# Kernel tuning notes

Measured on AMD Instinct MI355X. Metric: run time of the kernel, lower is better.

## Reference

```python
import jax, jax.numpy as jnp
import numpy as np

B, L, D = 4, 2048, 256
H, HD = 8, 64
MAX_LEN = 2048


def setup_inputs() -> dict:
    key = jax.random.key(0)
    ks = jax.random.split(key, 5)
    x = jax.random.normal(ks[0], (B, L, D), dtype=jnp.float32)
    glorot_q = (2.0 / (D + H * HD)) ** 0.5
    Wq = jax.random.normal(ks[1], (D, H * HD), dtype=jnp.float32) * glorot_q
    Wk = jax.random.normal(ks[2], (D, H * HD), dtype=jnp.float32) * glorot_q
    bq = jnp.zeros((H, 1, 1, HD), dtype=jnp.float32)
    bk = jnp.zeros((H, 1, 1, HD), dtype=jnp.float32)
    prior_mean = jax.random.uniform(ks[3], (H,), dtype=jnp.float32, minval=-1.0, maxval=1.0)
    log_prior_std = jnp.full((H,), np.log(0.4), dtype=jnp.float32)
    return {"x": x, "Wq": Wq, "bq": bq, "Wk": Wk, "bk": bk,
            "prior_mean": prior_mean, "log_prior_std": log_prior_std,
            "max_length": MAX_LEN}


def _gaussian(x, mean, std):
    return 1.0 / std / jnp.sqrt(2.0 * 3.1415926) * jnp.exp(-0.5 * (x - mean) ** 2 / std ** 2)


def reference(x, Wq, bq, Wk, bk, prior_mean, log_prior_std, max_length):
    b, l, d = x.shape
    h, hd = bq.shape[0], bq.shape[-1]
    # normalized signed distance matrix [l, l]
    r = jnp.arange(l, dtype=jnp.float32)
    dist = (r[None, :] - r[:, None]) / float(max_length)
    # projections -> [h, b, l, hd] (split heads along last dim, heads leading)
    q = (x @ Wq).reshape(b, l, h, hd).transpose(2, 0, 1, 3) + bq
    k = (x @ Wk).reshape(b, l, h, hd).transpose(2, 0, 1, 3) + bk
    # gaussian positional prior per head [h, l, l]
    prior = _gaussian(dist[None, :, :], prior_mean[:, None, None],
                      jnp.exp(log_prior_std)[:, None, None])
    # scaled QK^T * prior -> softmax over keys
    scores = jnp.einsum('hbqd,hbkd->hbqk', q, k) * (float(hd) ** -0.5)
    att = jax.nn.softmax(scores * prior[:, None, :, :], axis=-1)
    # distance-weighted reduction instead of V-matmul: [h, b, l] -> [b, l, h]
    distance = jnp.einsum('hbqk,qk->hbq', att, dist)
    return distance.transpose(1, 2, 0)
```

## Files before the change

kernel.cpp:

```cpp
#include <hip/hip_runtime.h>
#include <math.h>


#define B_  4
#define L_  2048
#define D_  256
#define H_  8
#define HD_ 64

typedef unsigned int u32;
typedef unsigned short u16;
typedef short bf16x8 __attribute__((ext_vector_type(8)));
typedef float f32x4  __attribute__((ext_vector_type(4)));

__device__ __forceinline__ u16 bf16rne(float v) {
    u32 u = __float_as_uint(v);
    return (u16)((u + 0x7fffu + ((u >> 16) & 1u)) >> 16);
}
__device__ __forceinline__ float bf2f(u16 h) { return __uint_as_float(((u32)h) << 16); }

#if __has_builtin(__builtin_amdgcn_exp2f)
__device__ __forceinline__ float fast_exp2(float x) { return __builtin_amdgcn_exp2f(x); }
#else
__device__ __forceinline__ float fast_exp2(float x) { return exp2f(x); }
#endif

__global__ __launch_bounds__(256, 4) void projB_kernel(
    const float* __restrict__ x,
    const float* __restrict__ Wq, const float* __restrict__ bq,
    const float* __restrict__ Wk, const float* __restrict__ bk,
    u16* __restrict__ Qhi, u16* __restrict__ Qlo,
    u16* __restrict__ Khi, u16* __restrict__ Klo)
{
    __shared__ __align__(16) u16 Bs[2][64][40];

    const int z = blockIdx.z;
    const float* W    = z ? Wk : Wq;
    const float* bias = z ? bk : bq;
    u16* Ohi = z ? Khi : Qhi;
    u16* Olo = z ? Klo : Qlo;

    const int t = threadIdx.x, w = t >> 6, l = t & 63;
    const int kc = l & 15, lhi = l >> 4;
    const int m0 = blockIdx.x * 128 + w * 32;
    const int h  = blockIdx.y;

    const float* xp0 = x + (size_t)(m0 + kc) * D_;
    const float* xp1 = x + (size_t)(m0 + 16 + kc) * D_;

    f32x4 acc[2][4];
    #pragma unroll
    for (int mf = 0; mf < 2; ++mf)
        #pragma unroll
        for (int nf = 0; nf < 4; ++nf) acc[mf][nf] = (f32x4){0.f, 0.f, 0.f, 0.f};

    for (int ks = 0; ks < 8; ++ks) {
        __syncthreads();
        #pragma unroll
        for (int j = 0; j < 2; ++j) {
            const int fid = t + j * 256;
            const int kr = fid >> 4, c4 = fid & 15;
            float4 v = *(const float4*)&W[(size_t)(ks*32 + kr) * 512 + h*64 + c4*4];
            float vv[4] = {v.x, v.y, v.z, v.w};
            #pragma unroll
            for (int e = 0; e < 4; ++e) {
                const int n = c4*4 + e;
                const u16 hi = bf16rne(vv[e]);
                Bs[0][n][kr] = hi;
                Bs[1][n][kr] = bf16rne(vv[e] - bf2f(hi));
            }
        }
        __syncthreads();

        union { u16 u[8]; bf16x8 v; } ah[2], al[2];
        #pragma unroll
        for (int mf = 0; mf < 2; ++mf) {
            const float* xp = mf ? xp1 : xp0;
            float4 a = *(const float4*)(xp + ks*32 + lhi*8);
            float4 b = *(const float4*)(xp + ks*32 + lhi*8 + 4);
            float vv[8] = {a.x, a.y, a.z, a.w, b.x, b.y, b.z, b.w};
            #pragma unroll
            for (int e = 0; e < 8; ++e) {
                const u16 hi = bf16rne(vv[e]);
                ah[mf].u[e] = hi;
                al[mf].u[e] = bf16rne(vv[e] - bf2f(hi));
            }
        }

        #pragma unroll
        for (int nf = 0; nf < 4; ++nf) {
            const bf16x8 bh = *(const bf16x8*)&Bs[0][nf*16 + kc][lhi*8];
            const bf16x8 bl = *(const bf16x8*)&Bs[1][nf*16 + kc][lhi*8];
            #pragma unroll
            for (int mf = 0; mf < 2; ++mf) {
                acc[mf][nf] = __builtin_amdgcn_mfma_f32_16x16x32_bf16(ah[mf].v, bh, acc[mf][nf], 0, 0, 0);
                acc[mf][nf] = __builtin_amdgcn_mfma_f32_16x16x32_bf16(ah[mf].v, bl, acc[mf][nf], 0, 0, 0);
                acc[mf][nf] = __builtin_amdgcn_mfma_f32_16x16x32_bf16(al[mf].v, bh, acc[mf][nf], 0, 0, 0);
            }
        }
    }

    #pragma unroll
    for (int mf = 0; mf < 2; ++mf)
        #pragma unroll
        for (int nf = 0; nf < 4; ++nf) {
            const float bv = bias[h * 64 + nf*16 + kc];
            #pragma unroll
            for (int r = 0; r < 4; ++r) {
                const float v = acc[mf][nf][r] + bv;
                const u16 hi = bf16rne(v);
                const u16 lo = bf16rne(v - bf2f(hi));
                const int m = m0 + mf*16 + lhi*4 + r;
                const int bb = m >> 11, ll = m & (L_ - 1);
                const size_t o = (((size_t)h * B_ + bb) * L_ + ll) * HD_ + nf*16 + kc;
                Ohi[o] = hi; Olo[o] = lo;
            }
        }
}

__global__ __launch_bounds__(512, 2) void attn_kernel(
    const u16* __restrict__ Qhi, const u16* __restrict__ Qlo,
    const u16* __restrict__ Khi, const u16* __restrict__ Klo,
    const float* __restrict__ prior_mean, const float* __restrict__ log_prior_std,
    const int* __restrict__ max_len, float* __restrict__ out)
{
    __shared__ __align__(16) u16 kls[2][2][64 * 64];

    const int t = threadIdx.x, w = t >> 6, l = t & 63;
    const int kc = l & 15, lhi = l >> 4;

    const int p = blockIdx.x;
    const int xcd = p & 7, s = p >> 3;
    const int hb = xcd * 4 + (s >> 3);
    const int q0 = (s & 7) * 256;
    const int h = hb >> 2, b = hb & 3;
    const int qw = q0 + w * 32;

    const float iml = 1.0f / (float)(*max_len);
    const float mu  = prior_mean[h];
    const float sg  = __expf(log_prior_std[h]);
    const float isg = 1.0f / sg;
    const float S2  = 0.84932180f;
    const float A2  = iml * isg * S2;
    const float B2  = -mu * isg * S2;
    const float LC  = __log2f(0.125f * 1.44269504089f / (sg * 2.5066282746310002f));

    bf16x8 qh[2][2], ql2[2][2];
    #pragma unroll
    for (int qf = 0; qf < 2; ++qf)
        #pragma unroll
        for (int dh = 0; dh < 2; ++dh) {
            const size_t qo = ((size_t)hb * L_ + qw + qf*16 + kc) * HD_ + dh*32 + lhi*8;
            qh[qf][dh]  = *(const bf16x8*)&Qhi[qo];
            ql2[qf][dh] = *(const bf16x8*)&Qlo[qo];
        }

    const int d0q0 = lhi*4 - (q0 + w*32 + kc);
    const int d0q1 = d0q0 - 16;

    const int spl = t >> 8;
    const int srow = (t & 255) >> 2;
    const int sq = t & 3;
    const int sr7 = srow & 7;
    const u16* Kg = (spl ? Klo : Khi) + ((size_t)hb * L_ + srow) * HD_ + sq * 16;
    const int p0 = ((sq*2)     ^ sr7) * 8;
    const int p1 = ((sq*2 + 1) ^ sr7) * 8;
    u16* wdst0 = &kls[0][spl][srow * 64];
    u16* wdst1 = &kls[1][spl][srow * 64];

    const int sl0 = (lhi ^ (kc & 7)) * 8;
    const int sl1 = ((4 + lhi) ^ (kc & 7)) * 8;

    float lv0 = 0.f, wv0 = 0.f, lv1 = 0.f, wv1 = 0.f;

    uint4 ra0, ra1, rb0, rb1;
    ra0 = *(const uint4*)Kg; ra1 = *(const uint4*)(Kg + 8);
    *(uint4*)&wdst0[p0] = ra0; *(uint4*)&wdst0[p1] = ra1;
    ra0 = *(const uint4*)(Kg + 4096); ra1 = *(const uint4*)(Kg + 4096 + 8);
    __syncthreads();

#define LOADT(RX0, RX1, TI) { const u16* src_ = Kg + (size_t)(TI) * 4096; \
    RX0 = *(const uint4*)src_; RX1 = *(const uint4*)(src_ + 8); }
#define WRT(DST, RX0, RX1) { *(uint4*)&DST[p0] = RX0; *(uint4*)&DST[p1] = RX1; }
#define CTILE(TI, BS) { \
    const u16* bh_ = &kls[BS][0][0]; const u16* bl_ = &kls[BS][1][0]; \
    f32x4 acc[4][2]; \
    _Pragma("unroll") for (int kf = 0; kf < 4; ++kf) { \
        acc[kf][0] = (f32x4){0.f,0.f,0.f,0.f}; acc[kf][1] = (f32x4){0.f,0.f,0.f,0.f}; } \
    __builtin_amdgcn_s_setprio(1); \
    _Pragma("unroll") for (int kf = 0; kf < 4; ++kf) { \
        const int rb_ = (kf*16 + kc) * 64; \
        const bf16x8 ah0 = *(const bf16x8*)&bh_[rb_ + sl0]; \
        const bf16x8 ah1 = *(const bf16x8*)&bh_[rb_ + sl1]; \
        const bf16x8 al0 = *(const bf16x8*)&bl_[rb_ + sl0]; \
        const bf16x8 al1 = *(const bf16x8*)&bl_[rb_ + sl1]; \
        _Pragma("unroll") for (int qf = 0; qf < 2; ++qf) { \
            acc[kf][qf] = __builtin_amdgcn_mfma_f32_16x16x32_bf16(ah0, qh[qf][0],  acc[kf][qf], 0, 0, 0); \
            acc[kf][qf] = __builtin_amdgcn_mfma_f32_16x16x32_bf16(ah1, qh[qf][1],  acc[kf][qf], 0, 0, 0); \
            acc[kf][qf] = __builtin_amdgcn_mfma_f32_16x16x32_bf16(ah0, ql2[qf][0], acc[kf][qf], 0, 0, 0); \
            acc[kf][qf] = __builtin_amdgcn_mfma_f32_16x16x32_bf16(ah1, ql2[qf][1], acc[kf][qf], 0, 0, 0); \
            acc[kf][qf] = __builtin_amdgcn_mfma_f32_16x16x32_bf16(al0, qh[qf][0],  acc[kf][qf], 0, 0, 0); \
            acc[kf][qf] = __builtin_amdgcn_mfma_f32_16x16x32_bf16(al1, qh[qf][1],  acc[kf][qf], 0, 0, 0); \
        } \
    } \
    __builtin_amdgcn_s_setprio(0); \
    _Pragma("unroll") for (int qf = 0; qf < 2; ++qf) { \
        const float dbf = (float)((TI)*64 + (qf ? d0q1 : d0q0)); \
        const float t2b = fmaf(dbf, A2, B2); \
        float S0 = 0.f, S1 = 0.f; \
        _Pragma("unroll") for (int kf = 0; kf < 4; ++kf) \
            _Pragma("unroll") for (int r = 0; r < 4; ++r) { \
                const int cc = kf*16 + r; \
                const float t2c = fmaf((float)cc, A2, t2b); \
                const float pr  = fast_exp2(fmaf(-t2c, t2c, LC)); \
                const float e   = fast_exp2(acc[kf][qf][r] * pr); \
                S0 += e; if (cc) S1 = fmaf(e, (float)cc, S1); \
            } \
        if (qf == 0) { lv0 += S0; wv0 = fmaf(dbf, S0, wv0 + S1); } \
        else         { lv1 += S0; wv1 = fmaf(dbf, S0, wv1 + S1); } \
    } \
}

    for (int kt = 0; kt < 32; kt += 2) {
        if (kt + 2 < 32) LOADT(rb0, rb1, kt + 2);
        WRT(wdst1, ra0, ra1);
        CTILE(kt, 0);
        __syncthreads();
        if (kt + 3 < 32) LOADT(ra0, ra1, kt + 3);
        if (kt + 2 < 32) WRT(wdst0, rb0, rb1);
        CTILE(kt + 1, 1);
        __syncthreads();
    }
#undef LOADT
#undef WRT
#undef CTILE

    lv0 += __shfl_xor(lv0, 16); wv0 += __shfl_xor(wv0, 16);
    lv0 += __shfl_xor(lv0, 32); wv0 += __shfl_xor(wv0, 32);
    lv1 += __shfl_xor(lv1, 16); wv1 += __shfl_xor(wv1, 16);
    lv1 += __shfl_xor(lv1, 32); wv1 += __shfl_xor(wv1, 32);

    if (lhi == 0) {
        const int q = qw + kc;
        out[((size_t)(b * L_ + q)) * H_ + h] = (wv0 * iml) / lv0;
    } else if (lhi == 1) {
        const int q = qw + 16 + kc;
        out[((size_t)(b * L_ + q)) * H_ + h] = (wv1 * iml) / lv1;
    }
}

extern "C" void kernel_launch(void* const* d_in, const int* in_sizes, int n_in,
                              void* d_out, int out_size, void* d_ws, size_t ws_size,
                              hipStream_t stream)
{
    const float* x   = (const float*)d_in[0];
    const float* Wq  = (const float*)d_in[1];
    const float* bq  = (const float*)d_in[2];
    const float* Wk  = (const float*)d_in[3];
    const float* bk  = (const float*)d_in[4];
    const float* pm  = (const float*)d_in[5];
    const float* lps = (const float*)d_in[6];
    const int*   mlp = (const int*)d_in[7];
    float* out = (float*)d_out;

    u16* Qhi = (u16*)d_ws;
    u16* Qlo = Qhi + 4194304;
    u16* Khi = Qlo + 4194304;
    u16* Klo = Khi + 4194304;

    projB_kernel<<<dim3(64, 8, 2), 256, 0, stream>>>(x, Wq, bq, Wk, bk,
                                                     Qhi, Qlo, Khi, Klo);
    attn_kernel<<<dim3(256), 512, 0, stream>>>(Qhi, Qlo, Khi, Klo, pm, lps, mlp, out);
}
```

Baseline: 169.5 us.

## Split key range across two wave groups and double grid size

Each 512-thread block now handles 128 queries instead of 256. The block's two 4-wave groups each process alternating halves of the key tiles, and their softmax partial sums are combined through shared memory at the end. The grid doubles to 512 blocks and launch bounds ask for 4 blocks per CU, which raises occupancy and parallelism on the 256-CU device. In exchange, Q fragments are loaded twice as often, there is an extra reduction with a barrier, and register pressure is tighter under the stricter launch bound.

```diff
diff --git a/kernel.cpp b/kernel.cpp
--- a/kernel.cpp
+++ b/kernel.cpp
@@ -118,23 +118,26 @@
         }
 }
 
-__global__ __launch_bounds__(512, 2) void attn_kernel(
+__global__ __launch_bounds__(512, 4) void attn_kernel(
     const u16* __restrict__ Qhi, const u16* __restrict__ Qlo,
     const u16* __restrict__ Khi, const u16* __restrict__ Klo,
     const float* __restrict__ prior_mean, const float* __restrict__ log_prior_std,
     const int* __restrict__ max_len, float* __restrict__ out)
 {
-    __shared__ __align__(16) u16 kls[2][2][64 * 64];
+    __shared__ __align__(16) u16 kls[2][2][2][4096];
+    __shared__ float2 red2[2][128];
 
     const int t = threadIdx.x, w = t >> 6, l = t & 63;
     const int kc = l & 15, lhi = l >> 4;
+    const int kg = w >> 2;
+    const int w4 = w & 3;
 
     const int p = blockIdx.x;
     const int xcd = p & 7, s = p >> 3;
-    const int hb = xcd * 4 + (s >> 3);
-    const int q0 = (s & 7) * 256;
+    const int hb = xcd * 4 + (s >> 4);
+    const int q0 = (s & 15) * 128;
     const int h = hb >> 2, b = hb & 3;
-    const int qw = q0 + w * 32;
+    const int qw = q0 + w4 * 32;
 
     const float iml = 1.0f / (float)(*max_len);
     const float mu  = prior_mean[h];
@@ -155,35 +158,35 @@
             ql2[qf][dh] = *(const bf16x8*)&Qlo[qo];
         }
 
-    const int d0q0 = lhi*4 - (q0 + w*32 + kc);
+    const int d0q0 = lhi*4 - (qw + kc);
     const int d0q1 = d0q0 - 16;
 
-    const int spl = t >> 8;
-    const int srow = (t & 255) >> 2;
-    const int sq = t & 3;
-    const int sr7 = srow & 7;
-    const u16* Kg = (spl ? Klo : Khi) + ((size_t)hb * L_ + srow) * HD_ + sq * 16;
-    const int p0 = ((sq*2)     ^ sr7) * 8;
-    const int p1 = ((sq*2 + 1) ^ sr7) * 8;
-    u16* wdst0 = &kls[0][spl][srow * 64];
-    u16* wdst1 = &kls[1][spl][srow * 64];
+    const int tl  = t & 255;
+    const int spl = tl >> 7;
+    const int row = (tl & 127) >> 1;
+    const int sq  = tl & 1;
+    const int sr7 = row & 7;
+    const u16* Kg = (spl ? Klo : Khi) + ((size_t)hb * L_ + row) * HD_ + sq * 32;
+    u16* wdst0 = &kls[kg][0][spl][row * 64];
+    u16* wdst1 = &kls[kg][1][spl][row * 64];
 
     const int sl0 = (lhi ^ (kc & 7)) * 8;
     const int sl1 = ((4 + lhi) ^ (kc & 7)) * 8;
 
     float lv0 = 0.f, wv0 = 0.f, lv1 = 0.f, wv1 = 0.f;
 
-    uint4 ra0, ra1, rb0, rb1;
-    ra0 = *(const uint4*)Kg; ra1 = *(const uint4*)(Kg + 8);
-    *(uint4*)&wdst0[p0] = ra0; *(uint4*)&wdst0[p1] = ra1;
-    ra0 = *(const uint4*)(Kg + 4096); ra1 = *(const uint4*)(Kg + 4096 + 8);
-    __syncthreads();
-
-#define LOADT(RX0, RX1, TI) { const u16* src_ = Kg + (size_t)(TI) * 4096; \
-    RX0 = *(const uint4*)src_; RX1 = *(const uint4*)(src_ + 8); }
-#define WRT(DST, RX0, RX1) { *(uint4*)&DST[p0] = RX0; *(uint4*)&DST[p1] = RX1; }
-#define CTILE(TI, BS) { \
-    const u16* bh_ = &kls[BS][0][0]; const u16* bl_ = &kls[BS][1][0]; \
+    uint4 ra[4], rb[4];
+#define LOADT(RX, J) { const u16* src_ = Kg + (size_t)(2*(J) + kg) * 4096; \
+    RX[0] = *(const uint4*)src_;        RX[1] = *(const uint4*)(src_ + 8); \
+    RX[2] = *(const uint4*)(src_ + 16); RX[3] = *(const uint4*)(src_ + 24); }
+#define WRT(DST, RX) { \
+    *(uint4*)&DST[((sq*4 + 0) ^ sr7) * 8] = RX[0]; \
+    *(uint4*)&DST[((sq*4 + 1) ^ sr7) * 8] = RX[1]; \
+    *(uint4*)&DST[((sq*4 + 2) ^ sr7) * 8] = RX[2]; \
+    *(uint4*)&DST[((sq*4 + 3) ^ sr7) * 8] = RX[3]; }
+#define CTILE(J, BS) { \
+    const int TI_ = 2*(J) + kg; \
+    const u16* bh_ = &kls[kg][BS][0][0]; const u16* bl_ = &kls[kg][BS][1][0]; \
     f32x4 acc[4][2]; \
     _Pragma("unroll") for (int kf = 0; kf < 4; ++kf) { \
         acc[kf][0] = (f32x4){0.f,0.f,0.f,0.f}; acc[kf][1] = (f32x4){0.f,0.f,0.f,0.f}; } \
@@ -205,7 +208,7 @@
     } \
     __builtin_amdgcn_s_setprio(0); \
     _Pragma("unroll") for (int qf = 0; qf < 2; ++qf) { \
-        const float dbf = (float)((TI)*64 + (qf ? d0q1 : d0q0)); \
+        const float dbf = (float)(TI_*64 + (qf ? d0q1 : d0q0)); \
         const float t2b = fmaf(dbf, A2, B2); \
         float S0 = 0.f, S1 = 0.f; \
         _Pragma("unroll") for (int kf = 0; kf < 4; ++kf) \
@@ -221,14 +224,18 @@
     } \
 }
 
-    for (int kt = 0; kt < 32; kt += 2) {
-        if (kt + 2 < 32) LOADT(rb0, rb1, kt + 2);
-        WRT(wdst1, ra0, ra1);
-        CTILE(kt, 0);
-        __syncthreads();
-        if (kt + 3 < 32) LOADT(ra0, ra1, kt + 3);
-        if (kt + 2 < 32) WRT(wdst0, rb0, rb1);
-        CTILE(kt + 1, 1);
+    LOADT(ra, 0); WRT(wdst0, ra);
+    LOADT(ra, 1);
+    __syncthreads();
+
+    for (int j = 0; j < 16; j += 2) {
+        if (j + 2 < 16) LOADT(rb, j + 2);
+        WRT(wdst1, ra);
+        CTILE(j, 0);
+        __syncthreads();
+        if (j + 3 < 16) LOADT(ra, j + 3);
+        if (j + 2 < 16) WRT(wdst0, rb);
+        CTILE(j + 1, 1);
         __syncthreads();
     }
 #undef LOADT
@@ -240,12 +247,15 @@
     lv1 += __shfl_xor(lv1, 16); wv1 += __shfl_xor(wv1, 16);
     lv1 += __shfl_xor(lv1, 32); wv1 += __shfl_xor(wv1, 32);
 
-    if (lhi == 0) {
-        const int q = qw + kc;
-        out[((size_t)(b * L_ + q)) * H_ + h] = (wv0 * iml) / lv0;
-    } else if (lhi == 1) {
-        const int q = qw + 16 + kc;
-        out[((size_t)(b * L_ + q)) * H_ + h] = (wv1 * iml) / lv1;
+    if (lhi == 0)      red2[kg][w4*32 + kc]      = make_float2(lv0, wv0);
+    else if (lhi == 1) red2[kg][w4*32 + 16 + kc] = make_float2(lv1, wv1);
+    __syncthreads();
+
+    if (t < 128) {
+        const float2 a = red2[0][t], c = red2[1][t];
+        const float lv = a.x + c.x, wv = a.y + c.y;
+        const int q = q0 + t;
+        out[((size_t)(b * L_ + q)) * H_ + h] = (wv * iml) / lv;
     }
 }
 
@@ -270,5 +280,5 @@
 
     projB_kernel<<<dim3(64, 8, 2), 256, 0, stream>>>(x, Wq, bq, Wk, bk,
                                                      Qhi, Qlo, Khi, Klo);
-    attn_kernel<<<dim3(256), 512, 0, stream>>>(Qhi, Qlo, Khi, Klo, pm, lps, mlp, out);
-}
+    attn_kernel<<<dim3(512), 512, 0, stream>>>(Qhi, Qlo, Khi, Klo, pm, lps, mlp, out);
+}
```

Result: slower. 199.0 us (+17.4%).
